# Performance work log

Hardware: AMD Instinct MI355X
Metric: run time of the kernel (lower is better)

Reference implementation:

```python
import jax, jax.numpy as jnp
import numpy as np

D_MODEL = 1024
N_HEAD = 16
HEAD_SIZE = D_MODEL // N_HEAD
LAYER_ID = 12
N_LAYER = 24
HEAD_SIZE_DIVISOR = 8
TM_DIM = 32   # TIME_MIX_EXTRA_DIM
TD_DIM = 64   # TIME_DECAY_EXTRA_DIM
B, T = 4, 1024
EPS = 1e-5 * HEAD_SIZE_DIVISOR ** 2


def setup_inputs() -> dict:
    key = jax.random.key(0)
    ks = jax.random.split(key, 12)
    C = D_MODEL
    r0 = LAYER_ID / (N_LAYER - 1)
    r1 = 1.0 - LAYER_ID / N_LAYER
    ddd = np.arange(C, dtype=np.float64) / C
    time_maa_x = (1.0 - ddd ** r1).astype(np.float32)
    time_maa_w = (1.0 - ddd ** r1).astype(np.float32)
    time_maa_k = (1.0 - ddd ** r1).astype(np.float32)
    time_maa_v = (1.0 - (ddd ** r1 + 0.3 * r0)).astype(np.float32)
    time_maa_r = (1.0 - ddd ** (0.5 * r1)).astype(np.float32)
    time_maa_g = (1.0 - ddd ** (0.5 * r1)).astype(np.float32)
    n = np.arange(C, dtype=np.float64)
    time_decay = (-6.0 + 5.0 * (n / (C - 1)) ** (0.7 + 1.3 * r0)).astype(np.float32)
    zig = ((n + 1) % 3 - 1) * 0.1
    time_faaaa = (r0 * (1 - n / (C - 1)) + zig).astype(np.float32).reshape(N_HEAD, HEAD_SIZE)
    s = 1.0 / np.sqrt(C)
    inp = {
        "x": jax.random.normal(ks[0], (B, T, C), jnp.float32),
        "time_maa_x": jnp.asarray(time_maa_x),
        "time_maa_w": jnp.asarray(time_maa_w),
        "time_maa_k": jnp.asarray(time_maa_k),
        "time_maa_v": jnp.asarray(time_maa_v),
        "time_maa_r": jnp.asarray(time_maa_r),
        "time_maa_g": jnp.asarray(time_maa_g),
        "time_maa_w1": jax.random.uniform(ks[1], (C, TM_DIM * 5), jnp.float32, -0.01, 0.01),
        "time_maa_w2": jax.random.uniform(ks[2], (5, TM_DIM, C), jnp.float32, -0.01, 0.01),
        "time_decay": jnp.asarray(time_decay),
        "time_decay_w1": jax.random.uniform(ks[3], (C, TD_DIM), jnp.float32, -0.01, 0.01),
        "time_decay_w2": jax.random.uniform(ks[4], (TD_DIM, C), jnp.float32, -0.01, 0.01),
        "time_faaaa": jnp.asarray(time_faaaa),
        "W_r": jax.random.normal(ks[5], (C, C), jnp.float32) * s,
        "W_k": jax.random.normal(ks[6], (C, C), jnp.float32) * s,
        "W_v": jax.random.normal(ks[7], (C, C), jnp.float32) * s,
        "W_g": jax.random.normal(ks[8], (C, C), jnp.float32) * s,
        "W_o": jax.random.normal(ks[9], (C, C), jnp.float32) * s,
        "ln_gamma": jnp.ones((C,), jnp.float32),
        "ln_beta": jnp.zeros((C,), jnp.float32),
    }
    return inp


def _wkv6(r, k, v, w, u):
    # r,k,v,w: (B,T,H,K); u: (H,K). Sequential data-dependent linear attention.
    Bc, Tc, H, K = r.shape
    wdec = jnp.exp(-jnp.exp(w))  # decay in (0,1)

    def step(S, inp):
        r_t, k_t, v_t, wd_t = inp           # each (B,H,K)
        kv = k_t[:, :, :, None] * v_t[:, :, None, :]   # (B,H,K,K) key x value
        y = jnp.einsum('bhk,bhkj->bhj', r_t, S + u[None, :, :, None] * kv)
        S = S * wd_t[:, :, :, None] + kv    # decay along key dim, then accumulate
        return S, y

    S0 = jnp.zeros((Bc, H, K, K), r.dtype)
    xs = (jnp.swapaxes(r, 0, 1), jnp.swapaxes(k, 0, 1),
          jnp.swapaxes(v, 0, 1), jnp.swapaxes(wdec, 0, 1))
    _, ys = jax.lax.scan(step, S0, xs)      # ys: (T,B,H,K)
    return jnp.swapaxes(ys, 0, 1).reshape(Bc, Tc, H * K)


def reference(x, time_maa_x, time_maa_w, time_maa_k, time_maa_v, time_maa_r,
              time_maa_g, time_maa_w1, time_maa_w2, time_decay, time_decay_w1,
              time_decay_w2, time_faaaa, W_r, W_k, W_v, W_g, W_o, ln_gamma, ln_beta):
    Bc, Tc, C = x.shape
    H, K = N_HEAD, HEAD_SIZE
    # token shift: state[t] = x[t-1], zero at t=0
    xs = jnp.pad(x, ((0, 0), (1, 0), (0, 0)))[:, :-1]
    xx = xs - x
    # LoRA-style data-dependent mixing coefficients
    xxx = x + xx * time_maa_x
    m = jnp.tanh(xxx @ time_maa_w1).reshape(Bc, Tc, 5, TM_DIM)
    m = jnp.einsum('btfe,fec->fbtc', m, time_maa_w2)  # (5,B,T,C)
    mw, mk, mv, mr, mg = m[0], m[1], m[2], m[3], m[4]
    xw = x + xx * (time_maa_w + mw)
    xk = x + xx * (time_maa_k + mk)
    xv = x + xx * (time_maa_v + mv)
    xr = x + xx * (time_maa_r + mr)
    xg = x + xx * (time_maa_g + mg)
    r = xr @ W_r
    k = xk @ W_k
    v = xv @ W_v
    g = jax.nn.silu(xg @ W_g)
    w = time_decay + jnp.tanh(xw @ time_decay_w1) @ time_decay_w2
    y = _wkv6(r.reshape(Bc, Tc, H, K), k.reshape(Bc, Tc, H, K),
              v.reshape(Bc, Tc, H, K), w.reshape(Bc, Tc, H, K), time_faaaa)
    # GroupNorm with H groups over channel dim (per (b,t) position)
    yg = y.reshape(Bc, Tc, H, K)
    mu = jnp.mean(yg, axis=-1, keepdims=True)
    var = jnp.mean((yg - mu) ** 2, axis=-1, keepdims=True)
    yn = ((yg - mu) / jnp.sqrt(var + EPS)).reshape(Bc, Tc, C)
    yn = yn * ln_gamma + ln_beta
    return (yn * g) @ W_o
```

## Files before the change

### kernel.cpp

```cpp
#include <hip/hip_runtime.h>

#define Bb 4
#define Tt 1024
#define Cc 1024
#define Hh 16
#define BT (Bb*Tt)
#define CHUNK 32
#define NCH (Tt/CHUNK)

typedef unsigned int uint;
typedef unsigned short u16;
typedef __bf16 bf16x8 __attribute__((ext_vector_type(8)));
typedef float f32x4 __attribute__((ext_vector_type(4)));
typedef const __attribute__((address_space(1))) uint GU;
typedef __attribute__((address_space(3))) uint LU;

__device__ __forceinline__ float blo(uint u) { return __uint_as_float(u << 16); }
__device__ __forceinline__ float bhi(uint u) { return __uint_as_float(u & 0xffff0000u); }
__device__ __forceinline__ float b2f(u16 u) { return __uint_as_float(((uint)u) << 16); }
__device__ __forceinline__ u16 f2b(float f) {
  uint u = __float_as_uint(f);
  return (u16)((u + 0x7fffu + ((u >> 16) & 1u)) >> 16);
}

__global__ __launch_bounds__(256) void prep_xxx(const float* __restrict__ x,
    const float* __restrict__ maa_x, u16* __restrict__ xxx)
{
  int idx = blockIdx.x*256 + threadIdx.x;
  int c4 = idx & 255;
  int bt = idx >> 8;
  int t = bt & (Tt-1);
  float4 xc = ((const float4*)x)[idx];
  float4 xp = make_float4(0.f,0.f,0.f,0.f);
  if (t > 0) xp = ((const float4*)x)[idx - 256];
  float4 mx = ((const float4*)maa_x)[c4];
  ushort4 o;
  o.x = f2b(fmaf(xp.x - xc.x, mx.x, xc.x));
  o.y = f2b(fmaf(xp.y - xc.y, mx.y, xc.y));
  o.z = f2b(fmaf(xp.z - xc.z, mx.z, xc.z));
  o.w = f2b(fmaf(xp.w - xc.w, mx.w, xc.w));
  ((ushort4*)xxx)[idx] = o;
}

__global__ __launch_bounds__(256) void mix_mfma(
    const float* __restrict__ x, const float* __restrict__ m1p,
    const u16* __restrict__ w2T,
    const float* __restrict__ maa_w, const float* __restrict__ maa_k,
    const float* __restrict__ maa_v, const float* __restrict__ maa_r,
    const float* __restrict__ maa_g,
    u16* __restrict__ xw, u16* __restrict__ xk, u16* __restrict__ xv,
    u16* __restrict__ xr, u16* __restrict__ xg)
{
  const int tid = threadIdx.x;
  const int lane = tid & 63;
  const int wv = tid >> 6;
  const int sid = blockIdx.x*4 + wv;
  const int rs = sid >> 4, cs = sid & 15;
  const int r0 = rs*16, c0 = cs*64;
  const int fr = lane & 15, kc = lane >> 4;

  float xc[4][4], xd[4][4];
  #pragma unroll
  for (int n = 0; n < 4; ++n) {
    int col = c0 + n*16 + fr;
    #pragma unroll
    for (int q = 0; q < 4; ++q) {
      int row = r0 + kc*4 + q;
      size_t o = (size_t)row*Cc + col;
      float v = x[o];
      float p = ((row & (Tt-1)) != 0) ? x[o - Cc] : 0.f;
      xc[n][q] = v;
      xd[n][q] = p - v;
    }
  }

  const size_t aBase = (size_t)(r0 + fr)*160 + kc*8;
  u16* const outs[5] = {xw, xk, xv, xr, xg};
  const float* const maas[5] = {maa_w, maa_k, maa_v, maa_r, maa_g};

  #pragma unroll
  for (int f = 0; f < 5; ++f) {
    float s8[8] = {0.f,0.f,0.f,0.f,0.f,0.f,0.f,0.f};
    #pragma unroll
    for (int z = 0; z < 4; ++z) {
      const float4* p = (const float4*)(m1p + (size_t)z*655360 + aBase + f*32);
      float4 a = p[0], b = p[1];
      s8[0]+=a.x; s8[1]+=a.y; s8[2]+=a.z; s8[3]+=a.w;
      s8[4]+=b.x; s8[5]+=b.y; s8[6]+=b.z; s8[7]+=b.w;
    }
    u16 t8[8];
    #pragma unroll
    for (int j = 0; j < 8; ++j) t8[j] = f2b(tanhf(s8[j]));
    bf16x8 af = *(const bf16x8*)t8;
    f32x4 acc[4];
    #pragma unroll
    for (int n = 0; n < 4; ++n) {
      bf16x8 bg = *(const bf16x8*)(w2T + (size_t)(c0 + n*16 + fr)*160 + f*32 + kc*8);
      acc[n] = __builtin_amdgcn_mfma_f32_16x16x32_bf16(af, bg, f32x4{0.f,0.f,0.f,0.f}, 0, 0, 0);
    }
    const float* __restrict__ ma = maas[f];
    u16* __restrict__ op = outs[f];
    #pragma unroll
    for (int n = 0; n < 4; ++n) {
      int col = c0 + n*16 + fr;
      float mv = ma[col];
      #pragma unroll
      for (int q = 0; q < 4; ++q) {
        int row = r0 + kc*4 + q;
        op[(size_t)row*Cc + col] = f2b(fmaf(xd[n][q], mv + acc[n][q], xc[n][q]));
      }
    }
  }
}

struct WPair { const float* s; u16* d; int K; int N; };
struct WPack { WPair p[9]; };

__global__ __launch_bounds__(256) void transW(WPack wp) {
  WPair pr = wp.p[blockIdx.z];
  int c0 = blockIdx.x*32, r0 = blockIdx.y*32;
  if (c0 >= pr.N || r0 >= pr.K) return;
  __shared__ float tile[32][33];
  int tc = threadIdx.x & 31, tr = threadIdx.x >> 5;
  #pragma unroll
  for (int p = 0; p < 4; ++p)
    tile[tr + p*8][tc] = pr.s[(size_t)(r0 + tr + p*8)*pr.N + c0 + tc];
  __syncthreads();
  #pragma unroll
  for (int p = 0; p < 4; ++p) {
    int n = tr + p*8;
    pr.d[(size_t)(c0 + n)*pr.K + r0 + tc] = f2b(tile[tc][n]);
  }
}

template<bool OUTF32>
__device__ __forceinline__ void mfma_core(
    const u16* __restrict__ A, const u16* __restrict__ Bt,
    void* __restrict__ Cout, const float* __restrict__ bias,
    int ld, int kloop, int N, int act)
{
  __shared__ __align__(16) u16 lds[2][2][128*32];
  const int tid = threadIdx.x;
  const int lane = tid & 63;
  const int wv = __builtin_amdgcn_readfirstlane(tid >> 6);

  const int nby8 = gridDim.y >> 3;
  const int i_lin = blockIdx.y * gridDim.x + blockIdx.x;
  const int cx = i_lin & 7, rest = i_lin >> 3;
  const int bm = (cx * nby8 + rest % nby8) * 128;
  const int bn = (rest / nby8) * 128;

  const int wm = (wv >> 1) * 64;
  const int wn = (wv & 1) * 64;
  const int kc = lane >> 4;
  const int fr = lane & 15;

  const int srow = wv*16 + (lane >> 2);
  const int ssw  = (srow >> 1) & 3;
  const int scol = ((lane & 3) ^ ssw) * 8;
  const size_t aoff = (size_t)(bm + srow) * ld + scol;
  const size_t boff = (size_t)(bn + srow) * ld + scol;

#define STAGE(bufi, kt) do { \
    size_t ko_ = (size_t)(kt) * 32; \
    __builtin_amdgcn_global_load_lds((GU*)(A + aoff + ko_), \
        (LU*)&lds[bufi][0][wv*512], 16, 0, 0); \
    __builtin_amdgcn_global_load_lds((GU*)(A + aoff + (size_t)64*ld + ko_), \
        (LU*)&lds[bufi][0][wv*512 + 64*32], 16, 0, 0); \
    __builtin_amdgcn_global_load_lds((GU*)(Bt + boff + ko_), \
        (LU*)&lds[bufi][1][wv*512], 16, 0, 0); \
    __builtin_amdgcn_global_load_lds((GU*)(Bt + boff + (size_t)64*ld + ko_), \
        (LU*)&lds[bufi][1][wv*512 + 64*32], 16, 0, 0); \
  } while(0)

  int ard[4], brd[4];
  #pragma unroll
  for (int m = 0; m < 4; ++m) {
    int ra = wm + m*16 + fr;
    int rb = wn + m*16 + fr;
    ard[m] = ra*32 + (kc ^ ((ra >> 1) & 3))*8;
    brd[m] = rb*32 + (kc ^ ((rb >> 1) & 3))*8;
  }

  f32x4 acc[4][4];
  #pragma unroll
  for (int m = 0; m < 4; ++m)
    #pragma unroll
    for (int n = 0; n < 4; ++n)
      acc[m][n] = f32x4{0.f, 0.f, 0.f, 0.f};

  const int NK = kloop >> 5;
  STAGE(0, 0);
  __syncthreads();
  int buf = 0;
  for (int kt = 0; kt < NK; ++kt) {
    if (kt + 1 < NK) STAGE(buf^1, kt+1);
    bf16x8 af[4], bg[4];
    #pragma unroll
    for (int m = 0; m < 4; ++m) af[m] = *(const bf16x8*)&lds[buf][0][ard[m]];
    #pragma unroll
    for (int n = 0; n < 4; ++n) bg[n] = *(const bf16x8*)&lds[buf][1][brd[n]];
    #pragma unroll
    for (int m = 0; m < 4; ++m)
      #pragma unroll
      for (int n = 0; n < 4; ++n)
        acc[m][n] = __builtin_amdgcn_mfma_f32_16x16x32_bf16(af[m], bg[n], acc[m][n], 0, 0, 0);
    __syncthreads();
    buf ^= 1;
  }
#undef STAGE

  const int orow = bm + wm + (lane >> 4) * 4;
  const int ocol = bn + wn + fr;
  #pragma unroll
  for (int m = 0; m < 4; ++m) {
    #pragma unroll
    for (int n = 0; n < 4; ++n) {
      int col = ocol + n*16;
      if (col < N) {
        float bs = bias ? bias[col] : 0.f;
        #pragma unroll
        for (int q = 0; q < 4; ++q) {
          float vv = acc[m][n][q] + bs;
          if (act == 1) vv = tanhf(vv);
          else if (act == 2) vv = vv / (1.f + __expf(-vv));
          else if (act == 3) vv = __expf(-__expf(vv));
          else if (act == 4) vv = __expf(vv);
          size_t off = (size_t)(orow + m*16 + q) * N + col;
          if (OUTF32) ((float*)Cout)[off] = vv;
          else ((u16*)Cout)[off] = f2b(vv);
        }
      }
    }
  }
}

template<int ACT, bool OUTF32>
__global__ __launch_bounds__(256) void gemm_mfma(
    const u16* __restrict__ A, const u16* __restrict__ Bt,
    void* __restrict__ Cout, const float* __restrict__ bias, int K, int N)
{
  mfma_core<OUTF32>(A, Bt, Cout, bias, K, K, N, ACT);
}

__global__ __launch_bounds__(256) void gemm_ksplit(
    const u16* __restrict__ A, const u16* __restrict__ Bt,
    float* __restrict__ Cp, int ld, int ksz, int N)
{
  const int z = blockIdx.z;
  mfma_core<true>(A + (size_t)z*ksz, Bt + (size_t)z*ksz,
                  Cp + (size_t)z*4096*N, nullptr, ld, ksz, N, 0);
}

__global__ __launch_bounds__(256) void gemm_ew64(
    const float* __restrict__ wl1p, const u16* __restrict__ Bt,
    const float* __restrict__ tdecay, float* __restrict__ ew)
{
  const int tid = threadIdx.x;
  const int lane = tid & 63;
  const int wv = tid >> 6;
  const int nby8 = gridDim.y >> 3;
  const int i_lin = blockIdx.y * gridDim.x + blockIdx.x;
  const int cx = i_lin & 7, rest = i_lin >> 3;
  const int bm = (cx * nby8 + rest % nby8) * 128;
  const int bn = (rest / nby8) * 128;
  const int wm = (wv >> 1) * 64;
  const int wn = (wv & 1) * 64;
  const int kc = lane >> 4;
  const int fr = lane & 15;

  bf16x8 af[4][2];
  #pragma unroll
  for (int m = 0; m < 4; ++m) {
    int row = bm + wm + m*16 + fr;
    #pragma unroll
    for (int ks = 0; ks < 2; ++ks) {
      size_t base = (size_t)row*64 + ks*32 + kc*8;
      float s8[8] = {0.f,0.f,0.f,0.f,0.f,0.f,0.f,0.f};
      #pragma unroll
      for (int z = 0; z < 4; ++z) {
        const float4* p = (const float4*)(wl1p + (size_t)z*262144 + base);
        float4 a = p[0], b = p[1];
        s8[0]+=a.x; s8[1]+=a.y; s8[2]+=a.z; s8[3]+=a.w;
        s8[4]+=b.x; s8[5]+=b.y; s8[6]+=b.z; s8[7]+=b.w;
      }
      u16 t8[8];
      #pragma unroll
      for (int j = 0; j < 8; ++j) t8[j] = f2b(tanhf(s8[j]));
      af[m][ks] = *(const bf16x8*)t8;
    }
  }

  f32x4 acc[4][4];
  #pragma unroll
  for (int m = 0; m < 4; ++m)
    #pragma unroll
    for (int n = 0; n < 4; ++n)
      acc[m][n] = f32x4{0.f,0.f,0.f,0.f};

  #pragma unroll
  for (int ks = 0; ks < 2; ++ks) {
    bf16x8 bg[4];
    #pragma unroll
    for (int n = 0; n < 4; ++n)
      bg[n] = *(const bf16x8*)(Bt + (size_t)(bn + wn + n*16 + fr)*64 + ks*32 + kc*8);
    #pragma unroll
    for (int m = 0; m < 4; ++m)
      #pragma unroll
      for (int n = 0; n < 4; ++n)
        acc[m][n] = __builtin_amdgcn_mfma_f32_16x16x32_bf16(af[m][ks], bg[n], acc[m][n], 0, 0, 0);
  }

  const int orow = bm + wm + kc*4;
  const int ocol = bn + wn + fr;
  #pragma unroll
  for (int n = 0; n < 4; ++n) {
    int col = ocol + n*16;
    float bs = tdecay[col];
    #pragma unroll
    for (int m = 0; m < 4; ++m)
      #pragma unroll
      for (int q = 0; q < 4; ++q)
        ew[(size_t)(orow + m*16 + q)*Cc + col] = __expf(acc[m][n][q] + bs);
  }
}

struct GPack { const u16* A[4]; const u16* B[4]; u16* C[4]; };

#define VMW(n) asm volatile("s_waitcnt vmcnt(" #n ")" ::: "memory")
#define LGKM0() asm volatile("s_waitcnt lgkmcnt(0)" ::: "memory")
#define SCHB() __builtin_amdgcn_sched_barrier(0)
#define HBAR() __builtin_amdgcn_s_barrier()

__global__ __launch_bounds__(512) void gemm_rkvg256(GPack gp) {
  __shared__ __align__(16) u16 lds[2][2][2][8192];
  const int z = blockIdx.z;
  const u16* __restrict__ Ap  = gp.A[z];
  const u16* __restrict__ Btp = gp.B[z];
  u16* __restrict__ Cp = gp.C[z];
  const int act = (z == 3) ? 2 : 0;

  const int tid = threadIdx.x;
  const int lane = tid & 63;
  const int wv = __builtin_amdgcn_readfirstlane(tid >> 6);

  const int i_lin = blockIdx.y * gridDim.x + blockIdx.x;
  const int tile = (i_lin & 7) * 8 + (i_lin >> 3);
  const int bm = (tile >> 2) * 256;
  const int bn = (tile & 3) * 256;

  const int wm = (wv >> 2) * 128;
  const int wn = (wv & 3) * 64;
  const int kc = lane >> 4;
  const int fr = lane & 15;

  const int srow0 = (wv*2 + 0)*16 + (lane >> 2);
  const int srow1 = (wv*2 + 1)*16 + (lane >> 2);
  const int sc0 = ((lane & 3) ^ ((srow0 >> 1) & 3)) * 8;
  const int sc1 = ((lane & 3) ^ ((srow1 >> 1) & 3)) * 8;
  const size_t aoff0 = (size_t)(bm + srow0)*Cc + sc0;
  const size_t aoff1 = (size_t)(bm + srow1)*Cc + sc1;
  const size_t boff0 = (size_t)(bn + srow0)*Cc + sc0;
  const size_t boff1 = (size_t)(bn + srow1)*Cc + sc1;

  int ard[8], brd[4];
  #pragma unroll
  for (int mh = 0; mh < 2; ++mh)
    #pragma unroll
    for (int mf = 0; mf < 4; ++mf) {
      int r = wm + mh*64 + mf*16 + fr;
      ard[mh*4+mf] = r*32 + (kc ^ ((r >> 1) & 3))*8;
    }
  #pragma unroll
  for (int nf = 0; nf < 4; ++nf) {
    int r = wn + nf*16 + fr;
    brd[nf] = r*32 + (kc ^ ((r >> 1) & 3))*8;
  }

  f32x4 acc[8][4];
  #pragma unroll
  for (int m = 0; m < 8; ++m)
    #pragma unroll
    for (int n = 0; n < 4; ++n)
      acc[m][n] = f32x4{0.f, 0.f, 0.f, 0.f};

#define STG256(DB, MAT, KH, kt, off0, off1, src) do { \
    u16* dst_ = &lds[(DB)][(MAT)][(KH)][wv*1024]; \
    __builtin_amdgcn_global_load_lds((GU*)((src) + (off0) + (size_t)(kt)*64 + (KH)*32), \
        (LU*)dst_, 16, 0, 0); \
    __builtin_amdgcn_global_load_lds((GU*)((src) + (off1) + (size_t)(kt)*64 + (KH)*32), \
        (LU*)(dst_ + 512), 16, 0, 0); \
  } while(0)

#define PH256(cur, KH, MH, LOADB, STMAT, STKH, DOSTAGE, VMTOK) do { \
    _Pragma("unroll") \
    for (int mf = 0; mf < 4; ++mf) \
      af[mf] = *(const bf16x8*)&lds[(cur)][0][KH][ard[(MH)*4+mf]]; \
    if (LOADB) { \
      _Pragma("unroll") \
      for (int nf = 0; nf < 4; ++nf) \
        bg[nf] = *(const bf16x8*)&lds[(cur)][1][KH][brd[nf]]; \
    } \
    if (DOSTAGE) { \
      if ((STMAT) == 0) STG256((cur)^1, 0, STKH, t+1, aoff0, aoff1, Ap); \
      else              STG256((cur)^1, 1, STKH, t+1, boff0, boff1, Btp); \
    } \
    VMTOK; \
    SCHB(); \
    HBAR(); \
    LGKM0(); \
    SCHB(); \
    __builtin_amdgcn_s_setprio(1); \
    _Pragma("unroll") \
    for (int mf = 0; mf < 4; ++mf) \
      _Pragma("unroll") \
      for (int nf = 0; nf < 4; ++nf) \
        acc[(MH)*4+mf][nf] = __builtin_amdgcn_mfma_f32_16x16x32_bf16(af[mf], bg[nf], acc[(MH)*4+mf][nf], 0, 0, 0); \
    __builtin_amdgcn_s_setprio(0); \
    SCHB(); \
    HBAR(); \
  } while(0)

  const int NK = Cc >> 6;

  STG256(0, 0, 0, 0, aoff0, aoff1, Ap);
  STG256(0, 1, 0, 0, boff0, boff1, Btp);
  STG256(0, 0, 1, 0, aoff0, aoff1, Ap);
  STG256(0, 1, 1, 0, boff0, boff1, Btp);
  VMW(4);
  SCHB();
  HBAR();

  bf16x8 af[4], bg[4];
  int t;
  #pragma unroll 2
  for (t = 0; t < NK - 1; ++t) {
    const int cur = t & 1;
    PH256(cur, 0, 0, true,  0, 0, true,  (void)0);
    PH256(cur, 0, 1, false, 1, 0, true,  VMW(4));
    PH256(cur, 1, 0, true,  0, 1, true,  (void)0);
    PH256(cur, 1, 1, false, 1, 1, true,  VMW(4));
  }
  {
    const int cur = t & 1;
    PH256(cur, 0, 0, true,  0, 0, false, (void)0);
    PH256(cur, 0, 1, false, 0, 0, false, VMW(0));
    PH256(cur, 1, 0, true,  0, 0, false, (void)0);
    PH256(cur, 1, 1, false, 0, 0, false, (void)0);
  }
#undef PH256
#undef STG256

  const int orow = bm + wm + (lane >> 4) * 4;
  const int ocol = bn + wn + fr;
  #pragma unroll
  for (int m = 0; m < 8; ++m) {
    #pragma unroll
    for (int nf = 0; nf < 4; ++nf) {
      #pragma unroll
      for (int q = 0; q < 4; ++q) {
        float vv = acc[m][nf][q];
        if (act == 2) vv = vv / (1.f + __expf(-vv));
        Cp[(size_t)(orow + (m >> 2)*64 + (m & 3)*16 + q) * Cc + ocol + nf*16] = f2b(vv);
      }
    }
  }
}

__global__ __launch_bounds__(256) void wkv_pass1(u16* __restrict__ r,
    const u16* __restrict__ k, const u16* __restrict__ v,
    const float* __restrict__ ew, const float* __restrict__ u,
    float* __restrict__ y, u16* __restrict__ S, float* __restrict__ D)
{
  __shared__ __align__(16) u16 rS[CHUNK][72];
  __shared__ __align__(16) u16 kS[CHUNK][72];
  __shared__ __align__(16) u16 vS[CHUNK][72];
  __shared__ __align__(16) float bufEW[CHUNK][68];
  __shared__ __align__(16) float eKnL[CHUNK][68];
  __shared__ __align__(16) u16 Rt[CHUNK][72];
  __shared__ __align__(16) u16 Kt[CHUNK][72];
  __shared__ __align__(16) u16 Ru[CHUNK][72];
  __shared__ __align__(16) u16 KhT[64][40];
  __shared__ __align__(16) u16 VT[64][40];
  __shared__ __align__(16) u16 A_lds[CHUNK][40];
  __shared__ float uL[64];
  __shared__ float Dl[64];

  const int blk = blockIdx.x;
  const int chunk = blk & (NCH-1);
  const int bh = blk >> 5;
  const int h = bh & (Hh-1);
  const int b = bh >> 4;
  const int tid = threadIdx.x;
  const int lane = tid & 63;
  const int wv = tid >> 6;
  const int fr = lane & 15;
  const int kc = lane >> 4;

  const size_t rowbase = ((size_t)(b*Tt + chunk*CHUNK))*Cc + h*64;
  {
    int tt = tid >> 3, c8 = (tid & 7)*8;
    size_t go = rowbase + (size_t)tt*Cc + c8;
    *(uint4*)&rS[tt][c8] = *(const uint4*)(r + go);
    *(uint4*)&kS[tt][c8] = *(const uint4*)(k + go);
    *(uint4*)&vS[tt][c8] = *(const uint4*)(v + go);
    *(float4*)&bufEW[tt][c8]   = *(const float4*)(ew + go);
    *(float4*)&bufEW[tt][c8+4] = *(const float4*)(ew + go + 4);
  }
  if (tid < 64) uL[tid] = u[h*64 + tid];
  __syncthreads();

  if (tid < 64) {
    float lwp = 0.f;
    for (int t = 0; t < CHUNK; ++t) {
      float e = bufEW[t][tid];
      bufEW[t][tid] = __expf(lwp);
      lwp -= e;
      eKnL[t][tid] = __expf(-lwp);
    }
    Dl[tid] = __expf(lwp);
    D[(size_t)blk*64 + tid] = Dl[tid];
  }
  __syncthreads();

  {
    int t = tid >> 3, i0 = (tid & 7)*8;
    uint4 rv4 = *(const uint4*)&rS[t][i0];
    uint4 kv4 = *(const uint4*)&kS[t][i0];
    const uint* rw = (const uint*)&rv4;
    const uint* kw = (const uint*)&kv4;
    u16 rt8[8], kt8[8], ru8[8];
    #pragma unroll
    for (int q = 0; q < 8; ++q) {
      int i = i0 + q;
      float rv = (q & 1) ? bhi(rw[q>>1]) : blo(rw[q>>1]);
      float kv = (q & 1) ? bhi(kw[q>>1]) : blo(kw[q>>1]);
      float eR = bufEW[t][i];
      float eKn = eKnL[t][i];
      float ktv = kv * eKn;
      rt8[q] = f2b(rv * eR);
      kt8[q] = f2b(ktv);
      ru8[q] = f2b(rv * uL[i]);
      KhT[i][t] = f2b(ktv * Dl[i]);
      VT[i][t] = vS[t][i];
    }
    *(uint4*)&Rt[t][i0] = *(const uint4*)rt8;
    *(uint4*)&Kt[t][i0] = *(const uint4*)kt8;
    *(uint4*)&Ru[t][i0] = *(const uint4*)ru8;
  }
  __syncthreads();

  {
    const int wr = wv >> 1, wc = wv & 1;
    f32x4 accA = {0.f,0.f,0.f,0.f};
    f32x4 accD = {0.f,0.f,0.f,0.f};
    #pragma unroll
    for (int ks = 0; ks < 2; ++ks) {
      bf16x8 a  = *(const bf16x8*)&Rt[wr*16+fr][kc*8 + ks*32];
      bf16x8 bb = *(const bf16x8*)&Kt[wc*16+fr][kc*8 + ks*32];
      accA = __builtin_amdgcn_mfma_f32_16x16x32_bf16(a, bb, accA, 0, 0, 0);
      bf16x8 a2 = *(const bf16x8*)&Ru[wr*16+fr][kc*8 + ks*32];
      bf16x8 b2 = *(const bf16x8*)&kS[wc*16+fr][kc*8 + ks*32];
      accD = __builtin_amdgcn_mfma_f32_16x16x32_bf16(a2, b2, accD, 0, 0, 0);
    }
    #pragma unroll
    for (int q = 0; q < 4; ++q) {
      int trow = wr*16 + kc*4 + q;
      int scol = wc*16 + fr;
      float val = (scol < trow) ? accA[q] : ((scol == trow) ? accD[q] : 0.f);
      A_lds[trow][scol] = f2b(val);
    }
  }
  __syncthreads();

  #pragma unroll
  for (int tb = 0; tb < 2; ++tb) {
    bf16x8 a  = *(const bf16x8*)&A_lds[tb*16+fr][kc*8];
    bf16x8 bb = *(const bf16x8*)&VT[wv*16+fr][kc*8];
    f32x4 acc = {0.f,0.f,0.f,0.f};
    acc = __builtin_amdgcn_mfma_f32_16x16x32_bf16(a, bb, acc, 0, 0, 0);
    #pragma unroll
    for (int q = 0; q < 4; ++q) {
      int t = tb*16 + kc*4 + q;
      int j = wv*16 + fr;
      y[rowbase + (size_t)t*Cc + j] = acc[q];
    }
  }
  #pragma unroll
  for (int jb = 0; jb < 4; ++jb) {
    bf16x8 a  = *(const bf16x8*)&KhT[wv*16+fr][kc*8];
    bf16x8 bb = *(const bf16x8*)&VT[jb*16+fr][kc*8];
    f32x4 acc = {0.f,0.f,0.f,0.f};
    acc = __builtin_amdgcn_mfma_f32_16x16x32_bf16(a, bb, acc, 0, 0, 0);
    #pragma unroll
    for (int q = 0; q < 4; ++q) {
      int i = wv*16 + kc*4 + q;
      int j = jb*16 + fr;
      S[((size_t)blk*64 + i)*64 + j] = f2b(acc[q]);
    }
  }
  {
    int tt = tid >> 3, c8 = (tid & 7)*8;
    *(uint4*)(r + rowbase + (size_t)tt*Cc + c8) = *(const uint4*)&Rt[tt][c8];
  }
}

__global__ __launch_bounds__(256) void wkv_pass2(u16* __restrict__ S,
    const float* __restrict__ D)
{
  __shared__ float Dl[NCH][64];
  const int bh = blockIdx.x;
  const int tid = threadIdx.x;
  {
    const float4* src = (const float4*)(D + (size_t)bh*NCH*64);
    float4* dst = (float4*)&Dl[0][0];
    dst[tid] = src[tid];
    dst[tid + 256] = src[tid + 256];
  }
  __syncthreads();
  const int j = tid & 63, i0 = (tid >> 6)*16;
  float Sr[16];
  #pragma unroll
  for (int ii = 0; ii < 16; ++ii) Sr[ii] = 0.f;
  for (int c = 0; c < NCH; ++c) {
    size_t base = (((size_t)bh*NCH + c)*64 + i0)*64 + j;
    u16 tmp[16];
    #pragma unroll
    for (int ii = 0; ii < 16; ++ii) tmp[ii] = S[base + ii*64];
    #pragma unroll
    for (int ii = 0; ii < 16; ++ii) S[base + ii*64] = f2b(Sr[ii]);
    #pragma unroll
    for (int ii = 0; ii < 16; ++ii) Sr[ii] = fmaf(Sr[ii], Dl[c][i0+ii], b2f(tmp[ii]));
  }
}

__global__ __launch_bounds__(256) void gn_gate(const float* __restrict__ y,
   const u16* __restrict__ g, const u16* __restrict__ rc, const u16* __restrict__ S,
   const float* __restrict__ gamma, const float* __restrict__ beta, u16* __restrict__ out)
{
  __shared__ u16 rcl[8][Cc];
  const int bt0 = blockIdx.x * 8;
  const int b = bt0 >> 10;
  const int t0 = bt0 & (Tt-1);
  const int chunk = t0 >> 5;
  const int tid = threadIdx.x;
  #pragma unroll
  for (int rr = 0; rr < 8; ++rr)
    ((ushort4*)rcl[rr])[tid] = ((const ushort4*)(rc + (size_t)(bt0+rr)*Cc))[tid];
  __syncthreads();
  const int c0 = tid*4, h = c0 >> 6, j0 = c0 & 63;
  const u16* Sb = S + (((size_t)(b*Hh + h)*NCH + chunk)*64)*64 + j0;
  float corr[8][4];
  #pragma unroll
  for (int rr = 0; rr < 8; ++rr)
    #pragma unroll
    for (int q = 0; q < 4; ++q) corr[rr][q] = 0.f;
  #pragma unroll 4
  for (int i = 0; i < 64; ++i) {
    ushort4 sv = *(const ushort4*)(Sb + (size_t)i*64);
    float s0 = b2f(sv.x), s1 = b2f(sv.y), s2 = b2f(sv.z), s3 = b2f(sv.w);
    #pragma unroll
    for (int rr = 0; rr < 8; ++rr) {
      float rv = b2f(rcl[rr][h*64 + i]);
      corr[rr][0] = fmaf(rv, s0, corr[rr][0]);
      corr[rr][1] = fmaf(rv, s1, corr[rr][1]);
      corr[rr][2] = fmaf(rv, s2, corr[rr][2]);
      corr[rr][3] = fmaf(rv, s3, corr[rr][3]);
    }
  }
  float4 ga = ((const float4*)gamma)[tid];
  float4 be = ((const float4*)beta)[tid];
  #pragma unroll
  for (int rr = 0; rr < 8; ++rr) {
    size_t o4 = (size_t)(bt0+rr)*(Cc/4) + tid;
    float4 yv = ((const float4*)y)[o4];
    yv.x += corr[rr][0]; yv.y += corr[rr][1]; yv.z += corr[rr][2]; yv.w += corr[rr][3];
    float s  = yv.x + yv.y + yv.z + yv.w;
    float sq = yv.x*yv.x + yv.y*yv.y + yv.z*yv.z + yv.w*yv.w;
    #pragma unroll
    for (int m = 1; m < 16; m <<= 1) {
      s  += __shfl_xor(s, m, 64);
      sq += __shfl_xor(sq, m, 64);
    }
    float mu  = s * (1.f/64.f);
    float var = sq * (1.f/64.f) - mu*mu;
    float rstd = rsqrtf(var + 6.4e-4f);
    ushort4 gu = ((const ushort4*)g)[o4];
    ushort4 ou;
    ou.x = f2b(((yv.x - mu)*rstd*ga.x + be.x) * b2f(gu.x));
    ou.y = f2b(((yv.y - mu)*rstd*ga.y + be.y) * b2f(gu.y));
    ou.z = f2b(((yv.z - mu)*rstd*ga.z + be.z) * b2f(gu.z));
    ou.w = f2b(((yv.w - mu)*rstd*ga.w + be.w) * b2f(gu.w));
    ((ushort4*)out)[o4] = ou;
  }
}

extern "C" void kernel_launch(void* const* d_in, const int* in_sizes, int n_in,
                              void* d_out, int out_size, void* d_ws, size_t ws_size,
                              hipStream_t stream) {
  const float* x      = (const float*)d_in[0];
  const float* maa_x  = (const float*)d_in[1];
  const float* maa_w  = (const float*)d_in[2];
  const float* maa_k  = (const float*)d_in[3];
  const float* maa_v  = (const float*)d_in[4];
  const float* maa_r  = (const float*)d_in[5];
  const float* maa_g  = (const float*)d_in[6];
  const float* w1     = (const float*)d_in[7];
  const float* w2     = (const float*)d_in[8];
  const float* tdecay = (const float*)d_in[9];
  const float* tdw1   = (const float*)d_in[10];
  const float* tdw2   = (const float*)d_in[11];
  const float* faaaa  = (const float*)d_in[12];
  const float* Wr     = (const float*)d_in[13];
  const float* Wk     = (const float*)d_in[14];
  const float* Wv     = (const float*)d_in[15];
  const float* Wg     = (const float*)d_in[16];
  const float* Wo     = (const float*)d_in[17];
  const float* gamma  = (const float*)d_in[18];
  const float* beta   = (const float*)d_in[19];
  float* out = (float*)d_out;

  const size_t MB = 1u << 20;
  char* wsb = (char*)d_ws;
  float* ewb  = (float*)(wsb + 0);
  float* m1p  = (float*)(wsb + 0);
  u16*   w2T  = (u16*)(wsb + 12*MB);
  u16*   xk   = (u16*)(wsb + 16*MB);
  u16*   xv   = (u16*)(wsb + 24*MB);
  u16*   xr   = (u16*)(wsb + 32*MB);
  u16*   xg   = (u16*)(wsb + 40*MB);
  u16*   xw   = (u16*)(wsb + 48*MB);
  u16*   rbuf = (u16*)(wsb + 56*MB);
  float* wl1p = (float*)(wsb + 56*MB);
  u16*   kbuf = (u16*)(wsb + 64*MB);
  u16*   vbuf = (u16*)(wsb + 72*MB);
  u16*   gbuf = (u16*)(wsb + 80*MB);
  float* Dbuf = (float*)(wsb + 88*MB);
  u16*   Sbuf = (u16*)(wsb + 16*MB);
  u16*   BW0  = (u16*)(wsb + 88*MB + 512*1024);
  u16*   BW1  = (u16*)((char*)BW0 + 2*MB);
  u16*   BW2  = (u16*)((char*)BW1 + 2*MB);
  u16*   BW3  = (u16*)((char*)BW2 + 2*MB);
  u16*   BW4  = (u16*)((char*)BW3 + 2*MB);
  u16*   w1T  = (u16*)((char*)BW4 + 2*MB);
  u16*   tdw1T = (u16*)(wsb + 99*MB);
  u16*   tdw2T = (u16*)(wsb + 99*MB + 256*1024);
  u16*   gated = xr;
  u16*   xxx16 = (u16*)d_out;
  float* ybuf  = (float*)d_out;

  dim3 blk(256);
  WPack wp;
  wp.p[0] = {Wr, BW0, Cc, Cc};  wp.p[1] = {Wk, BW1, Cc, Cc};
  wp.p[2] = {Wv, BW2, Cc, Cc};  wp.p[3] = {Wg, BW3, Cc, Cc};
  wp.p[4] = {Wo, BW4, Cc, Cc};  wp.p[5] = {w1, w1T, Cc, 160};
  wp.p[6] = {tdw1, tdw1T, Cc, 64}; wp.p[7] = {tdw2, tdw2T, 64, Cc};
  wp.p[8] = {w2, w2T, 160, Cc};
  transW<<<dim3(32,32,9), blk, 0, stream>>>(wp);
  prep_xxx<<<BT*Cc/4/256, blk, 0, stream>>>(x, maa_x, xxx16);
  gemm_ksplit<<<dim3(2, 32, 4), blk, 0, stream>>>(xxx16, w1T, m1p, Cc, 256, 160);
  mix_mfma<<<1024, blk, 0, stream>>>(x, m1p, w2T, maa_w, maa_k, maa_v, maa_r, maa_g,
                                     xw, xk, xv, xr, xg);
  gemm_ksplit<<<dim3(1, 32, 4), blk, 0, stream>>>(xw, tdw1T, wl1p, Cc, 256, 64);
  gemm_ew64<<<dim3(8, 32), blk, 0, stream>>>(wl1p, tdw2T, tdecay, ewb);
  GPack gp;
  gp.A[0] = xr; gp.A[1] = xk; gp.A[2] = xv; gp.A[3] = xg;
  gp.B[0] = BW0; gp.B[1] = BW1; gp.B[2] = BW2; gp.B[3] = BW3;
  gp.C[0] = rbuf; gp.C[1] = kbuf; gp.C[2] = vbuf; gp.C[3] = gbuf;
  gemm_rkvg256<<<dim3(4, 16, 4), dim3(512), 0, stream>>>(gp);
  wkv_pass1<<<Bb*Hh*NCH, blk, 0, stream>>>(rbuf, kbuf, vbuf, ewb, faaaa, ybuf, Sbuf, Dbuf);
  wkv_pass2<<<Bb*Hh, blk, 0, stream>>>(Sbuf, Dbuf);
  gn_gate<<<BT/8, blk, 0, stream>>>(ybuf, gbuf, rbuf, Sbuf, gamma, beta, gated);
  gemm_mfma<0,true><<<dim3(8, 32), blk, 0, stream>>>(gated, BW4, out, nullptr, Cc, Cc);
}
```

Measured before the change: 200.3 us.

## Use fast tanh, LDS-staged coalesced stores, bf16 y buffer, multiplicative decay

Replaces tanhf with an exp-based fast tanh in the LoRA kernels. mix_mfma now stages its output tile through shared memory so each row goes out as 16-byte coalesced writes instead of scattered 2-byte stores. The wkv intra-chunk output y is stored as bf16 rather than fp32, halving that intermediate's traffic into gn_gate. The decay prefix becomes a running product with a reciprocal instead of repeated exp calls. These changes cost some precision in y, in the decay products and in tanh near saturation.

```diff
diff --git a/kernel.cpp b/kernel.cpp
--- a/kernel.cpp
+++ b/kernel.cpp
@@ -21,6 +21,10 @@
 __device__ __forceinline__ u16 f2b(float f) {
   uint u = __float_as_uint(f);
   return (u16)((u + 0x7fffu + ((u >> 16) & 1u)) >> 16);
+}
+__device__ __forceinline__ float fast_tanh(float x) {
+  float e = __expf(2.f * x);
+  return 1.f - 2.f / (e + 1.f);
 }
 
 __global__ __launch_bounds__(256) void prep_xxx(const float* __restrict__ x,
@@ -51,6 +55,7 @@
     u16* __restrict__ xw, u16* __restrict__ xk, u16* __restrict__ xv,
     u16* __restrict__ xr, u16* __restrict__ xg)
 {
+  __shared__ __align__(16) u16 strip[4][16][72];
   const int tid = threadIdx.x;
   const int lane = tid & 63;
   const int wv = tid >> 6;
@@ -90,7 +95,7 @@
     }
     u16 t8[8];
     #pragma unroll
-    for (int j = 0; j < 8; ++j) t8[j] = f2b(tanhf(s8[j]));
+    for (int j = 0; j < 8; ++j) t8[j] = f2b(fast_tanh(s8[j]));
     bf16x8 af = *(const bf16x8*)t8;
     f32x4 acc[4];
     #pragma unroll
@@ -102,13 +107,17 @@
     u16* __restrict__ op = outs[f];
     #pragma unroll
     for (int n = 0; n < 4; ++n) {
-      int col = c0 + n*16 + fr;
-      float mv = ma[col];
+      int colL = n*16 + fr;
+      float mv = ma[c0 + colL];
       #pragma unroll
-      for (int q = 0; q < 4; ++q) {
-        int row = r0 + kc*4 + q;
-        op[(size_t)row*Cc + col] = f2b(fmaf(xd[n][q], mv + acc[n][q], xc[n][q]));
-      }
+      for (int q = 0; q < 4; ++q)
+        strip[wv][kc*4 + q][colL] = f2b(fmaf(xd[n][q], mv + acc[n][q], xc[n][q]));
+    }
+    #pragma unroll
+    for (int rd = 0; rd < 2; ++rd) {
+      int r8 = (lane >> 3) + rd*8;
+      uint4 v = *(const uint4*)&strip[wv][r8][(lane & 7)*8];
+      *(uint4*)(op + (size_t)(r0 + r8)*Cc + c0 + (lane & 7)*8) = v;
     }
   }
 }
@@ -286,7 +295,7 @@
       }
       u16 t8[8];
       #pragma unroll
-      for (int j = 0; j < 8; ++j) t8[j] = f2b(tanhf(s8[j]));
+      for (int j = 0; j < 8; ++j) t8[j] = f2b(fast_tanh(s8[j]));
       af[m][ks] = *(const bf16x8*)t8;
     }
   }
@@ -470,7 +479,7 @@
 __global__ __launch_bounds__(256) void wkv_pass1(u16* __restrict__ r,
     const u16* __restrict__ k, const u16* __restrict__ v,
     const float* __restrict__ ew, const float* __restrict__ u,
-    float* __restrict__ y, u16* __restrict__ S, float* __restrict__ D)
+    u16* __restrict__ y, u16* __restrict__ S, float* __restrict__ D)
 {
   __shared__ __align__(16) u16 rS[CHUNK][72];
   __shared__ __align__(16) u16 kS[CHUNK][72];
@@ -511,15 +520,15 @@
   __syncthreads();
 
   if (tid < 64) {
-    float lwp = 0.f;
+    float eR = 1.f;
     for (int t = 0; t < CHUNK; ++t) {
       float e = bufEW[t][tid];
-      bufEW[t][tid] = __expf(lwp);
-      lwp -= e;
-      eKnL[t][tid] = __expf(-lwp);
-    }
-    Dl[tid] = __expf(lwp);
-    D[(size_t)blk*64 + tid] = Dl[tid];
+      bufEW[t][tid] = eR;
+      eR *= __expf(-e);
+      eKnL[t][tid] = __builtin_amdgcn_rcpf(eR);
+    }
+    Dl[tid] = eR;
+    D[(size_t)blk*64 + tid] = eR;
   }
   __syncthreads();
 
@@ -583,7 +592,7 @@
     for (int q = 0; q < 4; ++q) {
       int t = tb*16 + kc*4 + q;
       int j = wv*16 + fr;
-      y[rowbase + (size_t)t*Cc + j] = acc[q];
+      y[rowbase + (size_t)t*Cc + j] = f2b(acc[q]);
     }
   }
   #pragma unroll
@@ -634,7 +643,7 @@
   }
 }
 
-__global__ __launch_bounds__(256) void gn_gate(const float* __restrict__ y,
+__global__ __launch_bounds__(256) void gn_gate(const u16* __restrict__ y,
    const u16* __restrict__ g, const u16* __restrict__ rc, const u16* __restrict__ S,
    const float* __restrict__ gamma, const float* __restrict__ beta, u16* __restrict__ out)
 {
@@ -673,10 +682,13 @@
   #pragma unroll
   for (int rr = 0; rr < 8; ++rr) {
     size_t o4 = (size_t)(bt0+rr)*(Cc/4) + tid;
-    float4 yv = ((const float4*)y)[o4];
-    yv.x += corr[rr][0]; yv.y += corr[rr][1]; yv.z += corr[rr][2]; yv.w += corr[rr][3];
-    float s  = yv.x + yv.y + yv.z + yv.w;
-    float sq = yv.x*yv.x + yv.y*yv.y + yv.z*yv.z + yv.w*yv.w;
+    ushort4 yv4 = ((const ushort4*)y)[o4];
+    float y0 = b2f(yv4.x) + corr[rr][0];
+    float y1 = b2f(yv4.y) + corr[rr][1];
+    float y2 = b2f(yv4.z) + corr[rr][2];
+    float y3 = b2f(yv4.w) + corr[rr][3];
+    float s  = y0 + y1 + y2 + y3;
+    float sq = y0*y0 + y1*y1 + y2*y2 + y3*y3;
     #pragma unroll
     for (int m = 1; m < 16; m <<= 1) {
       s  += __shfl_xor(s, m, 64);
@@ -687,10 +699,10 @@
     float rstd = rsqrtf(var + 6.4e-4f);
     ushort4 gu = ((const ushort4*)g)[o4];
     ushort4 ou;
-    ou.x = f2b(((yv.x - mu)*rstd*ga.x + be.x) * b2f(gu.x));
-    ou.y = f2b(((yv.y - mu)*rstd*ga.y + be.y) * b2f(gu.y));
-    ou.z = f2b(((yv.z - mu)*rstd*ga.z + be.z) * b2f(gu.z));
-    ou.w = f2b(((yv.w - mu)*rstd*ga.w + be.w) * b2f(gu.w));
+    ou.x = f2b(((y0 - mu)*rstd*ga.x + be.x) * b2f(gu.x));
+    ou.y = f2b(((y1 - mu)*rstd*ga.y + be.y) * b2f(gu.y));
+    ou.z = f2b(((y2 - mu)*rstd*ga.z + be.z) * b2f(gu.z));
+    ou.w = f2b(((y3 - mu)*rstd*ga.w + be.w) * b2f(gu.w));
     ((ushort4*)out)[o4] = ou;
   }
 }
@@ -747,7 +759,7 @@
   u16*   tdw2T = (u16*)(wsb + 99*MB + 256*1024);
   u16*   gated = xr;
   u16*   xxx16 = (u16*)d_out;
-  float* ybuf  = (float*)d_out;
+  u16*   yb16  = (u16*)d_out;
 
   dim3 blk(256);
   WPack wp;
@@ -768,8 +780,8 @@
   gp.B[0] = BW0; gp.B[1] = BW1; gp.B[2] = BW2; gp.B[3] = BW3;
   gp.C[0] = rbuf; gp.C[1] = kbuf; gp.C[2] = vbuf; gp.C[3] = gbuf;
   gemm_rkvg256<<<dim3(4, 16, 4), dim3(512), 0, stream>>>(gp);
-  wkv_pass1<<<Bb*Hh*NCH, blk, 0, stream>>>(rbuf, kbuf, vbuf, ewb, faaaa, ybuf, Sbuf, Dbuf);
+  wkv_pass1<<<Bb*Hh*NCH, blk, 0, stream>>>(rbuf, kbuf, vbuf, ewb, faaaa, yb16, Sbuf, Dbuf);
   wkv_pass2<<<Bb*Hh, blk, 0, stream>>>(Sbuf, Dbuf);
-  gn_gate<<<BT/8, blk, 0, stream>>>(ybuf, gbuf, rbuf, Sbuf, gamma, beta, gated);
+  gn_gate<<<BT/8, blk, 0, stream>>>(yb16, gbuf, rbuf, Sbuf, gamma, beta, gated);
   gemm_mfma<0,true><<<dim3(8, 32), blk, 0, stream>>>(gated, BW4, out, nullptr, Cc, Cc);
 }
```

New measurement: 200.3 us. Within noise of the previous version (-0.0%).
